# Kernel optimization log

Hardware: AMD Instinct MI355X
Metric: run time of the kernel (lower is better)

The kernel has to match this reference:

```python
import jax, jax.numpy as jnp
import numpy as np

B, HH, WW, C = 16, 64, 64, 256
HEADS, DIM_K, DIM_U, DIM_OUT = 4, 16, 1, 256
DIM_V = DIM_OUT // HEADS  # 64
R = 23
EPS = 1e-3  # keras BatchNormalization default epsilon


def setup_inputs() -> dict:
    key = jax.random.key(0)
    ks = jax.random.split(key, 14)
    def n(i, shape, s=1.0):
        return jax.random.normal(ks[i], shape, dtype=jnp.float32) * s
    def u(i, shape):
        return jax.random.uniform(ks[i], shape, jnp.float32, 0.5, 1.5)
    return {
        "x": n(0, (B, HH, WW, C)),
        "Wq": n(1, (C, DIM_K * HEADS), 0.05),
        "Wk": n(2, (C, DIM_K * DIM_U), 0.05),
        "Wv": n(3, (C, DIM_V * DIM_U), 0.05),
        "gamma_q": u(4, (DIM_K * HEADS,)),
        "beta_q": n(5, (DIM_K * HEADS,), 0.1),
        "mean_q": n(6, (DIM_K * HEADS,), 0.1),
        "var_q": u(7, (DIM_K * HEADS,)),
        "gamma_v": u(8, (DIM_V * DIM_U,)),
        "beta_v": n(9, (DIM_V * DIM_U,), 0.1),
        "mean_v": n(10, (DIM_V * DIM_U,), 0.1),
        "var_v": u(11, (DIM_V * DIM_U,)),
        "pos_w": n(12, (1, R, R, DIM_U, DIM_K), 0.05),  # DHWIO, depth dim = v
        "pos_b": jnp.zeros((DIM_K,), jnp.float32),
    }


def reference(x, Wq, Wk, Wv, gamma_q, beta_q, mean_q, var_q,
              gamma_v, beta_v, mean_v, var_v, pos_w, pos_b):
    b = x.shape[0]
    n_pos = HH * WW
    # 1x1 conv projections = channel matmuls
    q = jnp.einsum('bhwc,cd->bhwd', x, Wq)
    k = jnp.einsum('bhwc,cd->bhwd', x, Wk)
    v = jnp.einsum('bhwc,cd->bhwd', x, Wv)
    # BatchNorm (inference mode: moving stats)
    q = (q - mean_q) * jax.lax.rsqrt(var_q + EPS) * gamma_q + beta_q
    v = (v - mean_v) * jax.lax.rsqrt(var_v + EPS) * gamma_v + beta_v
    # rearranges
    q = q.reshape(b, n_pos, HEADS, DIM_K).transpose(0, 2, 3, 1)    # b h k n
    k = k.reshape(b, n_pos, DIM_U, DIM_K).transpose(0, 2, 3, 1)    # b u k n
    v4 = v.reshape(b, n_pos, DIM_U, DIM_V).transpose(0, 2, 3, 1)   # b u v n
    k = jax.nn.softmax(k, axis=-1)  # softmax over positions
    # content lambda
    Lc = jnp.einsum('bukm,buvm->bkv', k, v4)
    Yc = jnp.einsum('bhkn,bkv->bnhv', q, Lc)
    # positional lambda via local Conv3D over (v, hh, ww) with u channels
    v5 = v4.reshape(b, DIM_U, DIM_V, HH, WW).transpose(0, 2, 3, 4, 1)  # b v hh ww u
    Lp = jax.lax.conv_general_dilated(
        v5, pos_w, window_strides=(1, 1, 1), padding='SAME',
        dimension_numbers=('NDHWC', 'DHWIO', 'NDHWC')) + pos_b         # b v hh ww k
    Lp = Lp.transpose(0, 1, 4, 2, 3).reshape(b, DIM_V, DIM_K, n_pos)   # b v k n
    Yp = jnp.einsum('bhkn,bvkn->bnhv', q, Lp)
    Y = Yc + Yp                                                        # b n h v
    return Y.reshape(b, HH, WW, HEADS * DIM_V)
```

## Files before the change

kernel.cpp:

```cpp
#include <hip/hip_runtime.h>
#include <stdint.h>

typedef __bf16 bf16x8 __attribute__((ext_vector_type(8)));
typedef float  f32x4  __attribute__((ext_vector_type(4)));
typedef float  f32x16 __attribute__((ext_vector_type(16)));
typedef unsigned short u16;

#define WCT_OFF   0u
#define SC_OFF    73728u
#define SH_OFF    74304u
#define BST_OFF   75008u
#define ZB_OFF    524288u
#define MSUM_OFF  640256u
#define LCB_OFF   642304u
#define QP_OFF    707840u
#define KT_OFF    9096448u
#define VT_OFF    11193600u
#define P_OFF     19582208u

__global__ void kP(const float* Wq, const float* Wk, const float* Wv,
                   const float* gq, const float* bq, const float* mq, const float* vq,
                   const float* gv, const float* bv, const float* mv, const float* vvar,
                   const float* pw, char* ws) {
  int t = threadIdx.x;
  int blk = blockIdx.x;
  if (blk < 144) {
    int n = blk, c = t;
    float val;
    if (n < 64)      val = Wq[c * 64 + n];
    else if (n < 80) val = Wk[c * 16 + (n - 64)];
    else             val = Wv[c * 64 + (n - 80)];
    ((__bf16*)(ws + WCT_OFF))[n * 256 + c] = (__bf16)val;
  } else if (blk == 144) {
    if (t < 144) {
      float s, sh;
      if (t < 64)      { s = gq[t] * rsqrtf(vq[t] + 1e-3f); sh = bq[t] - mq[t] * s; }
      else if (t < 80) { s = 1.f; sh = 0.f; }
      else { int i = t - 80; s = gv[i] * rsqrtf(vvar[i] + 1e-3f); sh = bv[i] - mv[i] * s; }
      ((float*)(ws + SC_OFF))[t] = s;
      ((float*)(ws + SH_OFF))[t] = sh;
    }
    f32x4 fz;
    fz[0] = 0.f; fz[1] = 0.f; fz[2] = 0.f; fz[3] = 0.f;
    *(f32x4*)(ws + ZB_OFF + t * 16) = fz;
  } else {
    int dy = blk - 145;
    __bf16* bst = (__bf16*)(ws + BST_OFF) + dy * 8192;
    for (int i = 0; i < 32; ++i) {
      int idx = i * 256 + t;
      int nt = idx >> 10;
      int w2 = (idx >> 9) & 1;
      int l  = (idx >> 3) & 63;
      int e  = idx & 7;
      int n  = nt * 32 + (l & 31);
      int xr = n >> 4, kch = n & 15;
      int o1 = (2 * nt + 5) & ~7;
      int j  = o1 + w2 * 16 + (l >> 5) * 8 + e;
      int dxw = j - xr - 5;
      float val = (dxw >= 0 && dxw < 23) ? pw[(dy * 23 + dxw) * 16 + kch] : 0.f;
      bst[idx] = (__bf16)val;
    }
  }
}

__global__ __launch_bounds__(256) void kA(const float* x, char* ws) {
  __shared__ __align__(16) u16 qlds[64 * 72];
  int t = threadIdx.x, w = t >> 6, l = t & 63;
  int m0 = blockIdx.x * 64;
  int b = m0 >> 12;
  int posb = m0 & 4095;
  const __bf16* wct = (const __bf16*)(ws + WCT_OFF);
  const float* sc = (const float*)(ws + SC_OFF);
  const float* sh = (const float*)(ws + SH_OFF);
  __bf16* qp = (__bf16*)(ws + QP_OFF);
  __bf16* kt = (__bf16*)(ws + KT_OFF);
  __bf16* vt = (__bf16*)(ws + VT_OFF);

  int rl = l & 15;
  int kg = l >> 4;

  f32x4 acc[9];
#pragma unroll
  for (int nf = 0; nf < 9; ++nf)
#pragma unroll
    for (int q = 0; q < 4; ++q) acc[nf][q] = 0.f;

  for (int ks = 0; ks < 8; ++ks) {
    int m = m0 + w * 16 + rl;
    const float* xp = x + (size_t)m * 256 + ks * 32 + kg * 8;
    f32x4 v0 = *(const f32x4*)xp;
    f32x4 v1 = *(const f32x4*)(xp + 4);
    bf16x8 a;
    a[0] = (__bf16)v0[0]; a[1] = (__bf16)v0[1]; a[2] = (__bf16)v0[2]; a[3] = (__bf16)v0[3];
    a[4] = (__bf16)v1[0]; a[5] = (__bf16)v1[1]; a[6] = (__bf16)v1[2]; a[7] = (__bf16)v1[3];
#pragma unroll
    for (int nf = 0; nf < 9; ++nf) {
      bf16x8 bfr = *(const bf16x8*)(wct + (nf * 16 + rl) * 256 + ks * 32 + kg * 8);
      acc[nf] = __builtin_amdgcn_mfma_f32_16x16x32_bf16(a, bfr, acc[nf], 0, 0, 0);
    }
  }

#pragma unroll
  for (int nf = 0; nf < 9; ++nf) {
    int ch = nf * 16 + rl;
    float s = sc[ch], shv = sh[ch];
    int pbase = w * 16 + kg * 4;
    union { __bf16 h[4]; uint2 u; } pk;
#pragma unroll
    for (int r = 0; r < 4; ++r) pk.h[r] = (__bf16)(acc[nf][r] * s + shv);
    if (ch < 64) {
#pragma unroll
      for (int r = 0; r < 4; ++r)
        qlds[(pbase + r) * 72 + ch] = ((u16*)&pk.h[r])[0];
    } else if (ch < 80) {
      *(uint2*)(kt + (size_t)(b * 16 + ch - 64) * 4096 + posb + pbase) = pk.u;
    } else {
      *(uint2*)(vt + (size_t)(b * 64 + ch - 80) * 4096 + posb + pbase) = pk.u;
    }
  }
  __syncthreads();
#pragma unroll
  for (int i = 0; i < 2; ++i) {
    int chunk = t + i * 256;
    int row = chunk >> 3, seg = chunk & 7;
    bf16x8 vq_ = *(const bf16x8*)(qlds + row * 72 + seg * 8);
    *(bf16x8*)(qp + (size_t)(b * 4096 + posb + row) * 64 + seg * 8) = vq_;
  }
}

__global__ void kB1(char* ws) {
  __shared__ float red[256];
  int t = threadIdx.x;
  int b = blockIdx.x >> 4, kk = blockIdx.x & 15;
  const __bf16* kt = (const __bf16*)(ws + KT_OFF) + (size_t)(b * 16 + kk) * 4096;
  __bf16* P = (__bf16*)(ws + P_OFF) + (size_t)(b * 16 + kk) * 4096;
  float v[16];
  bf16x8 c0 = *(const bf16x8*)(kt + t * 16);
  bf16x8 c1 = *(const bf16x8*)(kt + t * 16 + 8);
#pragma unroll
  for (int i = 0; i < 8; ++i) { v[i] = (float)c0[i]; v[8 + i] = (float)c1[i]; }
  float mx = v[0];
#pragma unroll
  for (int i = 1; i < 16; ++i) mx = fmaxf(mx, v[i]);
  red[t] = mx; __syncthreads();
  for (int s = 128; s > 0; s >>= 1) { if (t < s) red[t] = fmaxf(red[t], red[t + s]); __syncthreads(); }
  mx = red[0]; __syncthreads();
  float se = 0.f;
  union { __bf16 h[8]; uint4 u; } p0, p1;
#pragma unroll
  for (int i = 0; i < 8; ++i) { float e = expf(v[i] - mx); se += e; p0.h[i] = (__bf16)e; }
#pragma unroll
  for (int i = 0; i < 8; ++i) { float e = expf(v[8 + i] - mx); se += e; p1.h[i] = (__bf16)e; }
  *(uint4*)(P + t * 16) = p0.u;
  *(uint4*)(P + t * 16 + 8) = p1.u;
  red[t] = se; __syncthreads();
  for (int s = 128; s > 0; s >>= 1) { if (t < s) red[t] += red[t + s]; __syncthreads(); }
  if (t == 0) {
    float* ms = (float*)(ws + MSUM_OFF);
    ms[(b * 16 + kk) * 2] = mx;
    ms[(b * 16 + kk) * 2 + 1] = 1.f / red[0];
  }
}

__global__ __launch_bounds__(256) void kB2(char* ws, const float* pos_b) {
  __shared__ float red[16][256];
  int t = threadIdx.x;
  int b = blockIdx.x >> 6, v = blockIdx.x & 63;
  const __bf16* P = (const __bf16*)(ws + P_OFF) + (size_t)b * 16 * 4096;
  const __bf16* vt = (const __bf16*)(ws + VT_OFF) + (size_t)(b * 64 + v) * 4096;
  const float* ms = (const float*)(ws + MSUM_OFF) + b * 32;
  float acc[16];
#pragma unroll
  for (int i = 0; i < 16; ++i) acc[i] = 0.f;
  for (int c = 0; c < 16; ++c) {
    int p = c * 256 + t;
    float vv = (float)vt[p];
#pragma unroll
    for (int i = 0; i < 16; ++i)
      acc[i] += (float)P[i * 4096 + p] * vv;
  }
#pragma unroll
  for (int i = 0; i < 16; ++i) red[i][t] = acc[i];
  __syncthreads();
  for (int s = 128; s > 0; s >>= 1) {
    if (t < s) {
#pragma unroll
      for (int i = 0; i < 16; ++i) red[i][t] += red[i][t + s];
    }
    __syncthreads();
  }
  if (t < 16) {
    float* lcb = (float*)(ws + LCB_OFF);
    lcb[(b * 16 + t) * 64 + v] = red[t][0] * ms[2 * t + 1] + pos_b[t];
  }
}

__global__ __launch_bounds__(512, 4) void kC(char* ws, float* out) {
  __shared__ __align__(16) u16 img[4][64][64];
  __shared__ __align__(16) u16 qt[2048];
  int t = threadIdx.x, w = t >> 6, l = t & 63;
  int bid = blockIdx.x;
  int swz = (bid & 7) * 256 + (bid >> 3);
  int b = swz >> 7;
  int rest = swz & 127;
  int yp = rest >> 2, xt = rest & 3;
  int y0 = yp * 2, x0g = xt * 16;
  const __bf16* vt  = (const __bf16*)(ws + VT_OFF);
  const __bf16* qp  = (const __bf16*)(ws + QP_OFF);
  const float*  lcb = (const float*)(ws + LCB_OFF) + b * 1024;
  const char*   bstc = (const char*)(ws + BST_OFF);
  const char*   zb   = (const char*)(ws + ZB_OFF) + (t & 255) * 16;

  int yy = w >> 2, ntp = w & 3;
  int hh = l >> 5;
  int o1_8 = ((4 * ntp + 5) & ~7) >> 3;

  int sv = t >> 3, sc8 = t & 7;
  int sgx = x0g - 16 + (sc8 ^ (sv & 7)) * 8;
  bool sokx = (sgx >= 0 && sgx < 64);
  const char* vsrc = (const char*)(vt + (size_t)(b * 64 + sv) * 4096 + sgx);

#define STAGE_IMG(slot, rowv) do {                                             \
    int _r = (rowv);                                                           \
    const char* _s = (sokx && _r >= 0 && _r < 64) ? (vsrc + _r * 128) : zb;    \
    __builtin_amdgcn_global_load_lds(                                          \
      (const __attribute__((address_space(1))) void*)_s,                       \
      (__attribute__((address_space(3))) void*)((char*)&img[0][0][0] + (slot) * 8192 + w * 1024), \
      16, 0, 0);                                                               \
  } while (0)

  STAGE_IMG(0, y0 - 11);
  STAGE_IMG(1, y0 - 10);
  STAGE_IMG(2, y0 - 9);
  {
    int f0 = t * 4;
    int qyy = f0 >> 10, qx = (f0 >> 6) & 15, qch = f0 & 63;
    *(uint2*)&qt[f0] =
      *(const uint2*)(qp + (size_t)(b * 4096 + (y0 + qyy) * 64 + x0g + qx) * 64 + qch);
  }
  asm volatile("s_waitcnt lgkmcnt(0)" ::: "memory");

  int afoff[2][2];
#pragma unroll
  for (int j = 0; j < 2; ++j)
#pragma unroll
    for (int w2 = 0; w2 < 2; ++w2)
      afoff[j][w2] = ((((2 * ntp + j) * 2 + w2) * 64) + l) * 16;

  f32x16 acc[2][2];
#pragma unroll
  for (int mf = 0; mf < 2; ++mf)
#pragma unroll
    for (int j = 0; j < 2; ++j)
#pragma unroll
      for (int q = 0; q < 16; ++q) acc[mf][j][q] = 0.f;

  for (int dy = 0; dy < 23; ++dy) {
    if (dy < 22) {
      asm volatile("s_waitcnt vmcnt(1)" ::: "memory");
    } else {
      asm volatile("s_waitcnt vmcnt(0)" ::: "memory");
    }
    __builtin_amdgcn_s_barrier();
    __builtin_amdgcn_sched_barrier(0);
    asm volatile("" ::: "memory");

    if (dy < 21) STAGE_IMG((dy + 3) & 3, y0 + dy - 8);

    const char* bdy = bstc + dy * 16384;
    bf16x8 af[2][2], bi[2][2];
#pragma unroll
    for (int j = 0; j < 2; ++j)
#pragma unroll
      for (int w2 = 0; w2 < 2; ++w2)
        af[j][w2] = *(const bf16x8*)(bdy + afoff[j][w2]);

    int rsl = (dy + yy) & 3;
#pragma unroll
    for (int mf = 0; mf < 2; ++mf) {
      int v = mf * 32 + (l & 31);
#pragma unroll
      for (int w2 = 0; w2 < 2; ++w2)
        bi[mf][w2] = *(const bf16x8*)(&img[rsl][v][((o1_8 + w2 * 2 + hh) ^ (v & 7)) * 8]);
    }
#pragma unroll
    for (int w2 = 0; w2 < 2; ++w2)
#pragma unroll
      for (int j = 0; j < 2; ++j) {
        acc[0][j] = __builtin_amdgcn_mfma_f32_32x32x16_bf16(af[j][w2], bi[0][w2], acc[0][j], 0, 0, 0);
        acc[1][j] = __builtin_amdgcn_mfma_f32_32x32x16_bf16(af[j][w2], bi[1][w2], acc[1][j], 0, 0, 0);
      }
  }
#undef STAGE_IMG

  float lc[2][16];
#pragma unroll
  for (int mf = 0; mf < 2; ++mf)
#pragma unroll
    for (int r = 0; r < 16; ++r) {
      int k = (r & 3) + 8 * ((r >> 2) & 1) + 4 * hh;
      lc[mf][r] = lcb[k * 64 + mf * 32 + (l & 31)];
    }
  size_t obase = ((size_t)b * 4096 + (y0 + yy) * 64 + x0g) * 256;
#pragma unroll
  for (int j = 0; j < 2; ++j) {
#pragma unroll
    for (int xh = 0; xh < 2; ++xh) {
      int x_local = 2 * (2 * ntp + j) + xh;
      const u16* qrow = &qt[(yy * 16 + x_local) * 64];
#pragma unroll
      for (int h = 0; h < 4; ++h) {
        float s0 = 0.f, s1 = 0.f;
#pragma unroll
        for (int r8 = 0; r8 < 8; ++r8) {
          int r = xh * 8 + r8;
          int k = (r8 & 3) + 8 * (r8 >> 2) + 4 * hh;
          float qv = (float)(*(const __bf16*)&qrow[h * 16 + k]);
          s0 += qv * (acc[0][j][r] + lc[0][r]);
          s1 += qv * (acc[1][j][r] + lc[1][r]);
        }
        s0 += __shfl_xor(s0, 32);
        s1 += __shfl_xor(s1, 32);
        float val = (l >= 32) ? s1 : s0;
        out[obase + (size_t)x_local * 256 + h * 64 + l] = val;
      }
    }
  }
}

extern "C" void kernel_launch(void* const* d_in, const int* in_sizes, int n_in,
                              void* d_out, int out_size, void* d_ws, size_t ws_size,
                              hipStream_t stream) {
  const float* x   = (const float*)d_in[0];
  const float* Wq  = (const float*)d_in[1];
  const float* Wk  = (const float*)d_in[2];
  const float* Wv  = (const float*)d_in[3];
  const float* gq  = (const float*)d_in[4];
  const float* bq  = (const float*)d_in[5];
  const float* mq  = (const float*)d_in[6];
  const float* vq  = (const float*)d_in[7];
  const float* gv  = (const float*)d_in[8];
  const float* bv  = (const float*)d_in[9];
  const float* mv  = (const float*)d_in[10];
  const float* vvr = (const float*)d_in[11];
  const float* pw  = (const float*)d_in[12];
  const float* pb  = (const float*)d_in[13];
  char* ws = (char*)d_ws;
  float* out = (float*)d_out;

  hipLaunchKernelGGL(kP, dim3(168), dim3(256), 0, stream,
                     Wq, Wk, Wv, gq, bq, mq, vq, gv, bv, mv, vvr, pw, ws);
  hipLaunchKernelGGL(kA, dim3(1024), dim3(256), 0, stream, x, ws);
  hipLaunchKernelGGL(kB1, dim3(256), dim3(256), 0, stream, ws);
  hipLaunchKernelGGL(kB2, dim3(1024), dim3(256), 0, stream, ws, pb);
  hipLaunchKernelGGL(kC, dim3(2048), dim3(512), 0, stream, ws, out);
}
```

Measured before the change: 173.1 us.

## Process two filter rows per barrier with a seven-slot LDS ring in kC

The positional-conv loop in kC now handles two dy rows per iteration. A 7-slot LDS image ring replaces the 4-slot one, and two rows are staged ahead with a vmcnt(2) wait. This halves the number of block-wide barriers and lets more MFMAs be issued between synchronisations. In exchange, LDS use per block grows from about 36KB to about 60KB, which may cut the number of blocks resident per CU below the launch-bounds target of 4.

```diff
diff --git a/kernel.cpp b/kernel.cpp
--- a/kernel.cpp
+++ b/kernel.cpp
@@ -196,7 +196,7 @@
 }
 
 __global__ __launch_bounds__(512, 4) void kC(char* ws, float* out) {
-  __shared__ __align__(16) u16 img[4][64][64];
+  __shared__ __align__(16) u16 img[7][64][64];
   __shared__ __align__(16) u16 qt[2048];
   int t = threadIdx.x, w = t >> 6, l = t & 63;
   int bid = blockIdx.x;
@@ -232,6 +232,8 @@
   STAGE_IMG(0, y0 - 11);
   STAGE_IMG(1, y0 - 10);
   STAGE_IMG(2, y0 - 9);
+  STAGE_IMG(3, y0 - 8);
+  STAGE_IMG(4, y0 - 7);
   {
     int f0 = t * 4;
     int qyy = f0 >> 10, qx = (f0 >> 6) & 15, qch = f0 & 63;
@@ -255,33 +257,82 @@
 #pragma unroll
       for (int q = 0; q < 16; ++q) acc[mf][j][q] = 0.f;
 
-  for (int dy = 0; dy < 23; ++dy) {
-    if (dy < 22) {
-      asm volatile("s_waitcnt vmcnt(1)" ::: "memory");
-    } else {
-      asm volatile("s_waitcnt vmcnt(0)" ::: "memory");
-    }
+  int sb = 0;
+  for (int i = 0; i < 11; ++i) {
+    int dy0 = 2 * i;
+    if (i < 10)      asm volatile("s_waitcnt vmcnt(2)" ::: "memory");
+    else             asm volatile("s_waitcnt vmcnt(1)" ::: "memory");
     __builtin_amdgcn_s_barrier();
     __builtin_amdgcn_sched_barrier(0);
     asm volatile("" ::: "memory");
 
-    if (dy < 21) STAGE_IMG((dy + 3) & 3, y0 + dy - 8);
-
-    const char* bdy = bstc + dy * 16384;
+    {
+      int sA = sb + 5; if (sA >= 7) sA -= 7;
+      int sB = sb + 6; if (sB >= 7) sB -= 7;
+      if (i <= 9) STAGE_IMG(sA, y0 + dy0 - 6);
+      if (i <= 8) STAGE_IMG(sB, y0 + dy0 - 5);
+    }
+
+    const char* bdy0 = bstc + dy0 * 16384;
+    bf16x8 af0[2][2], af1[2][2], bi0[2][2], bi1[2][2];
+#pragma unroll
+    for (int j = 0; j < 2; ++j)
+#pragma unroll
+      for (int w2 = 0; w2 < 2; ++w2) {
+        af0[j][w2] = *(const bf16x8*)(bdy0 + afoff[j][w2]);
+        af1[j][w2] = *(const bf16x8*)(bdy0 + 16384 + afoff[j][w2]);
+      }
+
+    int rA = sb + yy;     if (rA >= 7) rA -= 7;
+    int rB = sb + 1 + yy; if (rB >= 7) rB -= 7;
+#pragma unroll
+    for (int mf = 0; mf < 2; ++mf) {
+      int v = mf * 32 + (l & 31);
+      int sw = (v & 7);
+#pragma unroll
+      for (int w2 = 0; w2 < 2; ++w2) {
+        int c = ((o1_8 + w2 * 2 + hh) ^ sw) * 8;
+        bi0[mf][w2] = *(const bf16x8*)(&img[rA][v][c]);
+        bi1[mf][w2] = *(const bf16x8*)(&img[rB][v][c]);
+      }
+    }
+#pragma unroll
+    for (int w2 = 0; w2 < 2; ++w2)
+#pragma unroll
+      for (int j = 0; j < 2; ++j) {
+        acc[0][j] = __builtin_amdgcn_mfma_f32_32x32x16_bf16(af0[j][w2], bi0[0][w2], acc[0][j], 0, 0, 0);
+        acc[1][j] = __builtin_amdgcn_mfma_f32_32x32x16_bf16(af0[j][w2], bi0[1][w2], acc[1][j], 0, 0, 0);
+      }
+#pragma unroll
+    for (int w2 = 0; w2 < 2; ++w2)
+#pragma unroll
+      for (int j = 0; j < 2; ++j) {
+        acc[0][j] = __builtin_amdgcn_mfma_f32_32x32x16_bf16(af1[j][w2], bi1[0][w2], acc[0][j], 0, 0, 0);
+        acc[1][j] = __builtin_amdgcn_mfma_f32_32x32x16_bf16(af1[j][w2], bi1[1][w2], acc[1][j], 0, 0, 0);
+      }
+    sb += 2; if (sb >= 7) sb -= 7;
+  }
+
+  {
+    asm volatile("s_waitcnt vmcnt(0)" ::: "memory");
+    __builtin_amdgcn_s_barrier();
+    __builtin_amdgcn_sched_barrier(0);
+    asm volatile("" ::: "memory");
+    const char* bdy = bstc + 22 * 16384;
     bf16x8 af[2][2], bi[2][2];
 #pragma unroll
     for (int j = 0; j < 2; ++j)
 #pragma unroll
       for (int w2 = 0; w2 < 2; ++w2)
         af[j][w2] = *(const bf16x8*)(bdy + afoff[j][w2]);
-
-    int rsl = (dy + yy) & 3;
+    int rA = sb + yy; if (rA >= 7) rA -= 7;
 #pragma unroll
     for (int mf = 0; mf < 2; ++mf) {
       int v = mf * 32 + (l & 31);
+      int sw = (v & 7);
 #pragma unroll
       for (int w2 = 0; w2 < 2; ++w2)
-        bi[mf][w2] = *(const bf16x8*)(&img[rsl][v][((o1_8 + w2 * 2 + hh) ^ (v & 7)) * 8]);
+        bi[mf][w2] = *(const bf16x8*)(&img[rA][v][((o1_8 + w2 * 2 + hh) ^ sw) * 8]);
     }
 #pragma unroll
     for (int w2 = 0; w2 < 2; ++w2)
```

Measured after the change: 172.6 us, median of 2. Within noise of the previous version (-0.3%).
